# Optimization experiments

Hardware: AMD Instinct MI355X
Metric: run time of the kernel (lower is better)

The kernel has to match this reference:

```python
import math
import jax, jax.numpy as jnp
import numpy as np

DIM = 1024
FFN_DIM = 4096
NUM_HEADS = 16
HEAD_DIM = DIM // NUM_HEADS
SCALE = 1.0 / math.sqrt(HEAD_DIM)
EPS = 1e-5


def _layer_norm(x, gamma, beta):
    mu = jnp.mean(x, axis=-1, keepdims=True)
    var = jnp.mean(jnp.square(x - mu), axis=-1, keepdims=True)
    return (x - mu) * jax.lax.rsqrt(var + EPS) * gamma + beta


def _gelu_erf(x):
    # matches torch GELU module: x * 0.5 * (1 + erf(x / sqrt(2)))
    return x * 0.5 * (1.0 + jax.lax.erf(x / math.sqrt(2.0)))


def setup_inputs() -> dict:
    key = jax.random.key(0)
    ks = jax.random.split(key, 12)
    B, L = 2, 2048
    s = 0.02
    inp = {
        "x": jax.random.normal(ks[0], (B, L, DIM), dtype=jnp.float32),
        "g1": jnp.ones((DIM,), jnp.float32),
        "b1": jnp.zeros((DIM,), jnp.float32),
        "Wq": jax.random.normal(ks[1], (DIM, DIM), jnp.float32) * s,
        "bq": jnp.zeros((DIM,), jnp.float32),
        "Wk": jax.random.normal(ks[2], (DIM, DIM), jnp.float32) * s,
        "bk": jnp.zeros((DIM,), jnp.float32),
        "Wv": jax.random.normal(ks[3], (DIM, DIM), jnp.float32) * s,
        "bv": jnp.zeros((DIM,), jnp.float32),
        "Wo": jax.random.normal(ks[4], (DIM, DIM), jnp.float32) * s,
        "bo": jnp.zeros((DIM,), jnp.float32),
        "g2": jnp.ones((DIM,), jnp.float32),
        "b2": jnp.zeros((DIM,), jnp.float32),
        "W1": jax.random.normal(ks[5], (FFN_DIM, DIM), jnp.float32) * s,
        "bf1": jnp.zeros((FFN_DIM,), jnp.float32),
        "W2": jax.random.normal(ks[6], (DIM, FFN_DIM), jnp.float32) * s,
        "bf2": jnp.zeros((DIM,), jnp.float32),
    }
    return inp


def reference(x, g1, b1, Wq, bq, Wk, bk, Wv, bv, Wo, bo, g2, b2, W1, bf1, W2, bf2):
    B, L, C = x.shape
    n, c = NUM_HEADS, HEAD_DIM

    # ---- pre-norm self-attention ----
    h = _layer_norm(x, g1, b1)
    q = (h @ Wq.T + bq).reshape(B, L, n, c)
    k = (h @ Wk.T + bk).reshape(B, L, n, c)
    v = (h @ Wv.T + bv).reshape(B, L, n, c)
    attn = SCALE * jnp.einsum('binc,bjnc->bnij', q, k)   # [B, n, L, L]
    attn = jax.nn.softmax(attn, axis=-1)
    o = jnp.einsum('bnij,bjnc->binc', attn, v).reshape(B, L, C)
    x = x + (o @ Wo.T + bo)

    # ---- pre-norm FFN (GELU, erf form) ----
    h = _layer_norm(x, g2, b2)
    h = _gelu_erf(h @ W1.T + bf1)
    x = x + (h @ W2.T + bf2)
    return x
```

## Files before the change

### kernel.cpp

```cpp
#include <hip/hip_runtime.h>
#include <hip/hip_bf16.h>
#include <math.h>

typedef unsigned short u16;
typedef __attribute__((ext_vector_type(8))) __bf16 bf16x8;
typedef __attribute__((ext_vector_type(4))) float f32x4;

#define DIM   1024
#define LSEQ  2048
#define BTOK  4096
#define HD    64
#define FFN   4096
#define QSCL  0.18033688011112042f

#if __has_builtin(__builtin_amdgcn_exp2f)
#define EXP2(x) __builtin_amdgcn_exp2f(x)
#else
#define EXP2(x) exp2f(x)
#endif

__device__ __forceinline__ u16 f2bf(float f) {
  unsigned u = __builtin_bit_cast(unsigned, f);
  u += 0x7FFFu + ((u >> 16) & 1u);
  return (u16)(u >> 16);
}
__device__ __forceinline__ unsigned pk2(float a, float b) {
  return (unsigned)f2bf(a) | ((unsigned)f2bf(b) << 16);
}
__device__ __forceinline__ unsigned cvtpk(float lo, float hi) {
  unsigned r;
  asm("v_cvt_pk_bf16_f32 %0, %1, %2" : "=v"(r) : "v"(lo), "v"(hi));
  return r;
}
__device__ __forceinline__ f32x4 mfma16(bf16x8 a, bf16x8 b, f32x4 c) {
  return __builtin_amdgcn_mfma_f32_16x16x32_bf16(a, b, c, 0, 0, 0);
}
__device__ __forceinline__ void gload16(const void* g, void* l) {
  __builtin_amdgcn_global_load_lds((const __attribute__((address_space(1))) char*)g,
                                   (__attribute__((address_space(3))) char*)l, 16, 0, 0);
}
__device__ __forceinline__ float gelu_t(float v) {
  float v3 = v * v * v;
  float tt = fmaf(-0.10296766f, v3, -2.30258509f * v);
  return v * __builtin_amdgcn_rcpf(1.0f + EXP2(tt));
}

__global__ __launch_bounds__(256) void ln_kernel(const float* __restrict__ x,
                                                 const float* __restrict__ g,
                                                 const float* __restrict__ bta,
                                                 u16* __restrict__ out) {
  int row = blockIdx.x, t = threadIdx.x;
  const float* xr = x + (size_t)row * DIM;
  float4 xv = *(const float4*)(xr + t * 4);
  float s  = xv.x + xv.y + xv.z + xv.w;
  float ss = xv.x * xv.x + xv.y * xv.y + xv.z * xv.z + xv.w * xv.w;
#pragma unroll
  for (int m = 32; m >= 1; m >>= 1) {
    s  += __shfl_xor(s, m);
    ss += __shfl_xor(ss, m);
  }
  __shared__ float red[8];
  if ((t & 63) == 0) { red[(t >> 6) * 2] = s; red[(t >> 6) * 2 + 1] = ss; }
  __syncthreads();
  s  = red[0] + red[2] + red[4] + red[6];
  ss = red[1] + red[3] + red[5] + red[7];
  float mu  = s * (1.0f / DIM);
  float var = ss * (1.0f / DIM) - mu * mu;
  float rs  = rsqrtf(var + 1e-5f);
  float4 gv = *(const float4*)(g + t * 4);
  float4 bv = *(const float4*)(bta + t * 4);
  uint2 o;
  o.x = pk2((xv.x - mu) * rs * gv.x + bv.x, (xv.y - mu) * rs * gv.y + bv.y);
  o.y = pk2((xv.z - mu) * rs * gv.z + bv.z, (xv.w - mu) * rs * gv.w + bv.w);
  *(uint2*)(out + (size_t)row * DIM + t * 4) = o;
}

__global__ __launch_bounds__(256) void wcvt4(const float* __restrict__ Wq, const float* __restrict__ Wk,
                                             const float* __restrict__ Wv, const float* __restrict__ Wo,
                                             u16* __restrict__ dst) {
  int b = blockIdx.x;
  int r = b >> 9;
  const float* s = (r == 0) ? Wq : (r == 1) ? Wk : (r == 2) ? Wv : Wo;
  size_t i = (((size_t)(b & 511)) * 256 + threadIdx.x) * 8;
  float4 f0 = *(const float4*)(s + i), f1 = *(const float4*)(s + i + 4);
  uint4 o = { pk2(f0.x, f0.y), pk2(f0.z, f0.w), pk2(f1.x, f1.y), pk2(f1.z, f1.w) };
  *(uint4*)(dst + ((size_t)r << 20) + i) = o;
}
__global__ __launch_bounds__(256) void wcvt2(const float* __restrict__ W1, const float* __restrict__ W2,
                                             u16* __restrict__ d1, u16* __restrict__ d2) {
  int b = blockIdx.x;
  const float* s = (b < 2048) ? W1 : W2;
  u16* d = (b < 2048) ? d1 : d2;
  size_t i = (((size_t)(b & 2047)) * 256 + threadIdx.x) * 8;
  float4 f0 = *(const float4*)(s + i), f1 = *(const float4*)(s + i + 4);
  uint4 o = { pk2(f0.x, f0.y), pk2(f0.z, f0.w), pk2(f1.x, f1.y), pk2(f1.z, f1.w) };
  *(uint4*)(d + i) = o;
}

__global__ __launch_bounds__(256) void transpose_v(const u16* __restrict__ v,
                                                   u16* __restrict__ vt) {
  __shared__ u16 tls[64][80];
  int jb = blockIdx.x, bh = blockIdx.y, b = bh >> 4, h = bh & 15;
  int t = threadIdx.x;
  int r = t >> 2, seg = t & 3;
  const u16* src = v + (size_t)(b * LSEQ + jb * 64 + r) * DIM + h * HD + seg * 16;
  *(uint4*)&tls[r][seg * 16]     = *(const uint4*)src;
  *(uint4*)&tls[r][seg * 16 + 8] = *(const uint4*)(src + 8);
  __syncthreads();
  int c = t >> 2, jseg = t & 3;
  u16 tmp[16] __attribute__((aligned(16)));
#pragma unroll
  for (int i = 0; i < 16; i++) tmp[i] = tls[jseg * 16 + i][c];
  u16* dst = vt + ((size_t)bh * HD + c) * LSEQ + jb * 64 + jseg * 16;
  *(uint4*)dst       = *(const uint4*)tmp;
  *(uint4*)(dst + 8) = *(const uint4*)(tmp + 8);
}

struct GArg { const u16* Wb; const float* bias; u16* outB; float oscale; };

template <int EPI, int BM>
__global__ __launch_bounds__(256) void gemm3(const u16* __restrict__ A,
                                             GArg g0, GArg g1, GArg g2,
                                             const float* __restrict__ resid,
                                             float* __restrict__ outF,
                                             int N, int K, int nbPerW) {
  constexpr int WM = BM / 32;
  constexpr int ABUF = BM * 64;
  __shared__ u16 lsa[2][BM * 32];
  __shared__ u16 lsb[2][128 * 32];
  const int t = threadIdx.x;
  const int w = t >> 6, l = t & 63, l15 = l & 15, lg = l >> 4;
  const int wr = w >> 1, wc = w & 1;
  const int nwg = gridDim.x * gridDim.y;
  int flat = blockIdx.y * gridDim.x + blockIdx.x;
  flat = (flat & 7) * (nwg >> 3) + (flat >> 3);
  const int bx = flat % gridDim.x, by = flat / gridDim.x;
  const int sel = bx / nbPerW, nb = bx % nbPerW;
  GArg G = (sel == 0) ? g0 : ((sel == 1) ? g1 : g2);
  const int n0 = nb * 128, m0 = by * BM;

  f32x4 acc[WM][4];
#pragma unroll
  for (int m = 0; m < WM; m++)
#pragma unroll
    for (int n = 0; n < 4; n++) acc[m][n] = (f32x4){0.f, 0.f, 0.f, 0.f};

  const int grow = t >> 2;
  const int gcol = 8 * ((t & 3) ^ ((t >> 3) & 3));
  const u16* Asrc = A + (size_t)(m0 + grow) * K + gcol;
  const u16* Bsrc = G.Wb + (size_t)(n0 + grow) * K + gcol;
  const int rs = (l15 >> 1) & 3;

  const char* aadr = (const char*)lsa + (wr * (BM / 2) + l15) * 64 + (lg ^ rs) * 16;
  const char* badr = (const char*)lsb + (wc * 64 + l15) * 64 + (lg ^ rs) * 16;

  auto stage = [&](int k0, int buf) {
#pragma unroll
    for (int i = 0; i < BM / 64; i++)
      gload16(Asrc + (size_t)i * 64 * K + k0, (char*)lsa + buf * ABUF + i * 4096 + w * 1024);
#pragma unroll
    for (int i = 0; i < 2; i++)
      gload16(Bsrc + (size_t)i * 64 * K + k0, (char*)lsb + buf * 8192 + i * 4096 + w * 1024);
  };

  stage(0, 0);
  const int NT = K >> 5;
  for (int it = 0; it < NT; it++) {
    const int buf = it & 1;
    __syncthreads();
    if (it + 1 < NT) stage((it + 1) << 5, buf ^ 1);

    const char* ap = aadr + buf * ABUF;
    const char* bp = badr + buf * 8192;
    bf16x8 af[WM], bfr[4];
#pragma unroll
    for (int m = 0; m < WM; m++)
      af[m] = *(const bf16x8*)(ap + m * 1024);
#pragma unroll
    for (int n = 0; n < 4; n++)
      bfr[n] = *(const bf16x8*)(bp + n * 1024);
#pragma unroll
    for (int m = 0; m < WM; m++)
#pragma unroll
      for (int n = 0; n < 4; n++)
        acc[m][n] = mfma16(af[m], bfr[n], acc[m][n]);
  }

#pragma unroll
  for (int m = 0; m < WM; m++) {
    const int row = m0 + wr * (BM / 2) + m * 16 + lg * 4;
#pragma unroll
    for (int n = 0; n < 4; n++) {
      const int col = n0 + wc * 64 + n * 16 + l15;
      const float bias = G.bias[col];
#pragma unroll
      for (int r = 0; r < 4; r++) {
        const float v = acc[m][n][r] + bias;
        const size_t idx = (size_t)(row + r) * N + col;
        if (EPI == 0)      G.outB[idx] = f2bf(v * G.oscale);
        else if (EPI == 1) outF[idx] = v + resid[idx];
        else               G.outB[idx] = f2bf(gelu_t(v));
      }
    }
  }
}

__global__ __launch_bounds__(256, 4) void attn5(const u16* __restrict__ q,
                                                const u16* __restrict__ k,
                                                const u16* __restrict__ vt,
                                                u16* __restrict__ o) {
  __shared__ __align__(16) char smem[40960];
  const int t = threadIdx.x, w = t >> 6, l = t & 63, l15 = l & 15, lg = l >> 4;
  int flat = blockIdx.y * gridDim.x + blockIdx.x;
  flat = (flat & 7) * 128 + (flat >> 3);
  const int qbk = flat & 31, bh = flat >> 5;
  const int b = bh >> 4, h = bh & 15;
  const int qrow0 = b * LSEQ + qbk * 64 + w * 16;
  const int r7 = l15 & 7;
  const int c0 = lg ^ r7;

  bf16x8 av[2];
#pragma unroll
  for (int i = 0; i < 2; i++)
    av[i] = *(const bf16x8*)(q + (size_t)(qrow0 + l15) * DIM + h * HD + i * 32 + lg * 8);

  const char* adrA  = smem + l15 * 128 + c0 * 16;
  const char* adrB  = smem + l15 * 128 + (c0 ^ 4) * 16;
  const char* padrA = smem + 32768 + w * 2048 + l15 * 128 + c0 * 16;
  const char* padrB = smem + 32768 + w * 2048 + l15 * 128 + (c0 ^ 4) * 16;
  char* pwa[4];
#pragma unroll
  for (int cb = 0; cb < 4; cb++)
    pwa[cb] = smem + 32768 + w * 2048 + l15 * 128 +
              (((2 * cb + (lg >> 1)) ^ r7) * 16) + (lg & 1) * 8;

  const int grow = t >> 3, gchk = t & 7;
  const u16* ksrc = k + (size_t)(b * LSEQ + grow) * DIM + h * HD + 8 * (gchk ^ (grow & 7));
  const u16* vsrc = vt + ((size_t)bh * HD + grow) * LSEQ + 8 * (gchk ^ (grow & 7));

  f32x4 oacc[4];
#pragma unroll
  for (int cb = 0; cb < 4; cb++) oacc[cb] = (f32x4){0.f, 0.f, 0.f, 0.f};
  f32x4 minit = (f32x4){0.f, 0.f, 0.f, 0.f};
  float lsum = 0.f;

  auto issueTile = [&](int jt, int buf) {
    const u16* kp = ksrc + (size_t)jt * DIM;
    const u16* vp = vsrc + jt;
#pragma unroll
    for (int i = 0; i < 2; i++) {
      gload16(kp + (size_t)i * 32 * DIM,  smem + buf * 8192 + i * 4096 + w * 1024);
      gload16(vp + (size_t)i * 32 * LSEQ, smem + 16384 + buf * 8192 + i * 4096 + w * 1024);
    }
  };

  issueTile(0, 0);
  for (int it = 0; it < LSEQ / 64; it++) {
    const int buf = it & 1;
    __syncthreads();
    if (it + 1 < LSEQ / 64) issueTile((it + 1) * 64, buf ^ 1);
    const int ko = buf * 8192;

    f32x4 s[4];
    const char* kA = adrA + ko;
    const char* kB = adrB + ko;
    __builtin_amdgcn_s_setprio(1);
#pragma unroll
    for (int cb = 0; cb < 4; cb++) {
      bf16x8 kf0 = *(const bf16x8*)(kA + cb * 2048);
      bf16x8 kf1 = *(const bf16x8*)(kB + cb * 2048);
      s[cb] = mfma16(kf0, av[0], minit);
      s[cb] = mfma16(kf1, av[1], s[cb]);
    }
    __builtin_amdgcn_s_setprio(0);

    float tm = fmaxf(fmaxf(fmaxf(s[0][0], s[0][1]), fmaxf(s[0][2], s[0][3])),
                     fmaxf(fmaxf(fmaxf(s[1][0], s[1][1]), fmaxf(s[1][2], s[1][3])),
                           fmaxf(fmaxf(fmaxf(s[2][0], s[2][1]), fmaxf(s[2][2], s[2][3])),
                                 fmaxf(fmaxf(s[3][0], s[3][1]), fmaxf(s[3][2], s[3][3])))));
    if (__any(tm > 8.0f)) {
      float tr = fmaxf(tm, __shfl_xor(tm, 16));
      tr = fmaxf(tr, __shfl_xor(tr, 32));
      const float d = fmaxf(tr, 0.f);
      const float scl = EXP2(-d);
      const f32x4 dv = (f32x4){d, d, d, d};
      lsum *= scl;
      minit -= dv;
#pragma unroll
      for (int cb = 0; cb < 4; cb++) s[cb] -= dv;
#pragma unroll
      for (int r = 0; r < 4; r++) {
        const float so = __shfl(scl, lg * 4 + r);
#pragma unroll
        for (int cb = 0; cb < 4; cb++) oacc[cb][r] *= so;
      }
    }
    float ps = 0.f;
    uint2 pk[4];
#pragma unroll
    for (int cb = 0; cb < 4; cb++) {
      float a0 = EXP2(s[cb][0]);
      float a1 = EXP2(s[cb][1]);
      float a2 = EXP2(s[cb][2]);
      float a3 = EXP2(s[cb][3]);
      ps += (a0 + a1) + (a2 + a3);
      pk[cb].x = cvtpk(a0, a1);
      pk[cb].y = cvtpk(a2, a3);
    }
    lsum += ps;
#pragma unroll
    for (int cb = 0; cb < 4; cb++) *(uint2*)pwa[cb] = pk[cb];

    const char* vA = adrA + ko + 16384;
    const char* vB = adrB + ko + 16384;
    bf16x8 pa0 = *(const bf16x8*)padrA;
    bf16x8 pa1 = *(const bf16x8*)padrB;
    __builtin_amdgcn_s_setprio(1);
#pragma unroll
    for (int cb = 0; cb < 4; cb++) {
      bf16x8 vf0 = *(const bf16x8*)(vA + cb * 2048);
      oacc[cb] = mfma16(pa0, vf0, oacc[cb]);
    }
#pragma unroll
    for (int cb = 0; cb < 4; cb++) {
      bf16x8 vf1 = *(const bf16x8*)(vB + cb * 2048);
      oacc[cb] = mfma16(pa1, vf1, oacc[cb]);
    }
    __builtin_amdgcn_s_setprio(0);
  }

  float rl = lsum + __shfl_xor(lsum, 16);
  rl += __shfl_xor(rl, 32);
#pragma unroll
  for (int r = 0; r < 4; r++) {
    const float lo = __shfl(rl, lg * 4 + r);
    const float rcp = 1.0f / lo;
#pragma unroll
    for (int cb = 0; cb < 4; cb++) {
      o[(size_t)(qrow0 + lg * 4 + r) * DIM + h * HD + cb * 16 + l15] =
          f2bf(oacc[cb][r] * rcp);
    }
  }
}

extern "C" void kernel_launch(void* const* d_in, const int* in_sizes, int n_in,
                              void* d_out, int out_size, void* d_ws, size_t ws_size,
                              hipStream_t stream) {
  const float* x   = (const float*)d_in[0];
  const float* g1  = (const float*)d_in[1];
  const float* b1  = (const float*)d_in[2];
  const float* Wq  = (const float*)d_in[3];
  const float* bq  = (const float*)d_in[4];
  const float* Wk  = (const float*)d_in[5];
  const float* bk  = (const float*)d_in[6];
  const float* Wv  = (const float*)d_in[7];
  const float* bv  = (const float*)d_in[8];
  const float* Wo  = (const float*)d_in[9];
  const float* bo  = (const float*)d_in[10];
  const float* g2  = (const float*)d_in[11];
  const float* b2  = (const float*)d_in[12];
  const float* W1  = (const float*)d_in[13];
  const float* bf1 = (const float*)d_in[14];
  const float* W2  = (const float*)d_in[15];
  const float* bf2 = (const float*)d_in[16];
  float* out = (float*)d_out;

  const size_t E = (size_t)BTOK * DIM;
  u16* h     = (u16*)d_ws;
  u16* qb    = h + E;
  u16* kbuf  = qb + E;
  u16* vbuf  = kbuf + E;
  u16* vtb   = vbuf + E;
  u16* wqkvo = vtb + E;
  u16* ob    = vbuf;
  u16* W1b   = qb;
  u16* W2b   = kbuf;
  u16* mid   = vbuf;
  u16* h2    = h;
  float* x2  = out;

  u16* Wqb = wqkvo;
  u16* Wkb = wqkvo + ((size_t)1 << 20);
  u16* Wvb = wqkvo + ((size_t)2 << 20);
  u16* Wob = wqkvo + ((size_t)3 << 20);

  wcvt4<<<dim3(2048), dim3(256), 0, stream>>>(Wq, Wk, Wv, Wo, wqkvo);
  ln_kernel<<<dim3(BTOK), dim3(256), 0, stream>>>(x, g1, b1, h);
  gemm3<0, 128><<<dim3(24, BTOK / 128), 256, 0, stream>>>(
      h, GArg{Wqb, bq, qb, QSCL}, GArg{Wkb, bk, kbuf, 1.0f}, GArg{Wvb, bv, vbuf, 1.0f},
      nullptr, nullptr, DIM, DIM, 8);
  transpose_v<<<dim3(32, 32), 256, 0, stream>>>(vbuf, vtb);
  attn5<<<dim3(LSEQ / 64, 32), 256, 0, stream>>>(qb, kbuf, vtb, ob);
  {
    GArg s{Wob, bo, nullptr, 1.0f};
    gemm3<1, 64><<<dim3(8, BTOK / 64), 256, 0, stream>>>(ob, s, s, s, x, x2, DIM, DIM, 8);
  }
  wcvt2<<<dim3(4096), dim3(256), 0, stream>>>(W1, W2, W1b, W2b);
  ln_kernel<<<dim3(BTOK), dim3(256), 0, stream>>>(x2, g2, b2, h2);
  {
    GArg s{W1b, bf1, mid, 1.0f};
    gemm3<2, 128><<<dim3(32, BTOK / 128), 256, 0, stream>>>(h2, s, s, s, nullptr, nullptr, FFN, DIM, 32);
  }
  {
    GArg s{W2b, bf2, nullptr, 1.0f};
    gemm3<1, 64><<<dim3(8, BTOK / 64), 256, 0, stream>>>(mid, s, s, s, x2, out, DIM, FFN, 8);
  }
}
```

Measured before the change: 255.0 us.

## Deepen GEMM shared-memory pipeline to multi-stage with explicit vmcnt waits

```diff
diff --git a/kernel.cpp b/kernel.cpp
--- a/kernel.cpp
+++ b/kernel.cpp
@@ -118,16 +118,19 @@
 
 struct GArg { const u16* Wb; const float* bias; u16* outB; float oscale; };
 
-template <int EPI, int BM>
-__global__ __launch_bounds__(256) void gemm3(const u16* __restrict__ A,
+template <int EPI, int BM, int DEPTH>
+__global__ __launch_bounds__(256) void gemm4(const u16* __restrict__ A,
                                              GArg g0, GArg g1, GArg g2,
                                              const float* __restrict__ resid,
                                              float* __restrict__ outF,
                                              int N, int K, int nbPerW) {
-  constexpr int WM = BM / 32;
+  constexpr int WM  = BM / 32;
+  constexpr int LPT = BM / 64 + 2;
   constexpr int ABUF = BM * 64;
-  __shared__ u16 lsa[2][BM * 32];
-  __shared__ u16 lsb[2][128 * 32];
+  constexpr int BBUF = 8192;
+  constexpr int VX  = (DEPTH - 2) * LPT;
+  __shared__ u16 lsa[DEPTH][BM * 32];
+  __shared__ u16 lsb[DEPTH][128 * 32];
   const int t = threadIdx.x;
   const int w = t >> 6, l = t & 63, l15 = l & 15, lg = l >> 4;
   const int wr = w >> 1, wc = w & 1;
@@ -160,18 +163,23 @@
       gload16(Asrc + (size_t)i * 64 * K + k0, (char*)lsa + buf * ABUF + i * 4096 + w * 1024);
 #pragma unroll
     for (int i = 0; i < 2; i++)
-      gload16(Bsrc + (size_t)i * 64 * K + k0, (char*)lsb + buf * 8192 + i * 4096 + w * 1024);
+      gload16(Bsrc + (size_t)i * 64 * K + k0, (char*)lsb + buf * BBUF + i * 4096 + w * 1024);
   };
 
-  stage(0, 0);
+#pragma unroll
+  for (int p = 0; p < DEPTH - 1; p++) stage(p << 5, p);
+
   const int NT = K >> 5;
+  int bufR = 0, bufW = DEPTH - 1;
   for (int it = 0; it < NT; it++) {
-    const int buf = it & 1;
-    __syncthreads();
-    if (it + 1 < NT) stage((it + 1) << 5, buf ^ 1);
-
-    const char* ap = aadr + buf * ABUF;
-    const char* bp = badr + buf * 8192;
+    if constexpr (VX == 4) asm volatile("s_waitcnt vmcnt(4)" ::: "memory");
+    else if constexpr (VX == 6) asm volatile("s_waitcnt vmcnt(6)" ::: "memory");
+    else asm volatile("s_waitcnt vmcnt(0)" ::: "memory");
+    __builtin_amdgcn_s_barrier();
+    if (it + DEPTH - 1 < NT) stage((it + DEPTH - 1) << 5, bufW);
+
+    const char* ap = aadr + bufR * ABUF;
+    const char* bp = badr + bufR * BBUF;
     bf16x8 af[WM], bfr[4];
 #pragma unroll
     for (int m = 0; m < WM; m++)
@@ -179,11 +187,15 @@
 #pragma unroll
     for (int n = 0; n < 4; n++)
       bfr[n] = *(const bf16x8*)(bp + n * 1024);
+    __builtin_amdgcn_s_setprio(1);
 #pragma unroll
     for (int m = 0; m < WM; m++)
 #pragma unroll
       for (int n = 0; n < 4; n++)
         acc[m][n] = mfma16(af[m], bfr[n], acc[m][n]);
+    __builtin_amdgcn_s_setprio(0);
+    bufR = (bufR + 1 == DEPTH) ? 0 : bufR + 1;
+    bufW = (bufW + 1 == DEPTH) ? 0 : bufW + 1;
   }
 
 #pragma unroll
@@ -386,23 +398,23 @@
 
   wcvt4<<<dim3(2048), dim3(256), 0, stream>>>(Wq, Wk, Wv, Wo, wqkvo);
   ln_kernel<<<dim3(BTOK), dim3(256), 0, stream>>>(x, g1, b1, h);
-  gemm3<0, 128><<<dim3(24, BTOK / 128), 256, 0, stream>>>(
+  gemm4<0, 128, 3><<<dim3(24, BTOK / 128), 256, 0, stream>>>(
       h, GArg{Wqb, bq, qb, QSCL}, GArg{Wkb, bk, kbuf, 1.0f}, GArg{Wvb, bv, vbuf, 1.0f},
       nullptr, nullptr, DIM, DIM, 8);
   transpose_v<<<dim3(32, 32), 256, 0, stream>>>(vbuf, vtb);
   attn5<<<dim3(LSEQ / 64, 32), 256, 0, stream>>>(qb, kbuf, vtb, ob);
   {
     GArg s{Wob, bo, nullptr, 1.0f};
-    gemm3<1, 64><<<dim3(8, BTOK / 64), 256, 0, stream>>>(ob, s, s, s, x, x2, DIM, DIM, 8);
+    gemm4<1, 64, 4><<<dim3(8, BTOK / 64), 256, 0, stream>>>(ob, s, s, s, x, x2, DIM, DIM, 8);
   }
   wcvt2<<<dim3(4096), dim3(256), 0, stream>>>(W1, W2, W1b, W2b);
   ln_kernel<<<dim3(BTOK), dim3(256), 0, stream>>>(x2, g2, b2, h2);
   {
     GArg s{W1b, bf1, mid, 1.0f};
-    gemm3<2, 128><<<dim3(32, BTOK / 128), 256, 0, stream>>>(h2, s, s, s, nullptr, nullptr, FFN, DIM, 32);
+    gemm4<2, 128, 3><<<dim3(32, BTOK / 128), 256, 0, stream>>>(h2, s, s, s, nullptr, nullptr, FFN, DIM, 32);
   }
   {
     GArg s{W2b, bf2, nullptr, 1.0f};
-    gemm3<1, 64><<<dim3(8, BTOK / 64), 256, 0, stream>>>(mid, s, s, s, x2, out, DIM, FFN, 8);
-  }
-}
+    gemm4<1, 64, 4><<<dim3(8, BTOK / 64), 256, 0, stream>>>(mid, s, s, s, x2, out, DIM, FFN, 8);
+  }
+}
```

Result: no change. 258.7 us (+1.5%).

## Give each attention wave 32 query rows, halving waves per block

Applied to the files above, without the earlier changes.

```diff
diff --git a/kernel.cpp b/kernel.cpp
--- a/kernel.cpp
+++ b/kernel.cpp
@@ -205,7 +205,7 @@
   }
 }
 
-__global__ __launch_bounds__(256, 4) void attn5(const u16* __restrict__ q,
+__global__ __launch_bounds__(128, 2) void attn6(const u16* __restrict__ q,
                                                 const u16* __restrict__ k,
                                                 const u16* __restrict__ vt,
                                                 u16* __restrict__ o) {
@@ -215,42 +215,47 @@
   flat = (flat & 7) * 128 + (flat >> 3);
   const int qbk = flat & 31, bh = flat >> 5;
   const int b = bh >> 4, h = bh & 15;
-  const int qrow0 = b * LSEQ + qbk * 64 + w * 16;
+  const int qrow0 = b * LSEQ + qbk * 64 + w * 32;
   const int r7 = l15 & 7;
   const int c0 = lg ^ r7;
 
-  bf16x8 av[2];
-#pragma unroll
-  for (int i = 0; i < 2; i++)
-    av[i] = *(const bf16x8*)(q + (size_t)(qrow0 + l15) * DIM + h * HD + i * 32 + lg * 8);
+  bf16x8 av[2][2];
+#pragma unroll
+  for (int m = 0; m < 2; m++)
+#pragma unroll
+    for (int i = 0; i < 2; i++)
+      av[m][i] = *(const bf16x8*)(q + (size_t)(qrow0 + m * 16 + l15) * DIM + h * HD + i * 32 + lg * 8);
 
   const char* adrA  = smem + l15 * 128 + c0 * 16;
   const char* adrB  = smem + l15 * 128 + (c0 ^ 4) * 16;
-  const char* padrA = smem + 32768 + w * 2048 + l15 * 128 + c0 * 16;
-  const char* padrB = smem + 32768 + w * 2048 + l15 * 128 + (c0 ^ 4) * 16;
+  const char* padrA = smem + 32768 + w * 4096 + l15 * 128 + c0 * 16;
+  const char* padrB = smem + 32768 + w * 4096 + l15 * 128 + (c0 ^ 4) * 16;
   char* pwa[4];
 #pragma unroll
   for (int cb = 0; cb < 4; cb++)
-    pwa[cb] = smem + 32768 + w * 2048 + l15 * 128 +
+    pwa[cb] = smem + 32768 + w * 4096 + l15 * 128 +
               (((2 * cb + (lg >> 1)) ^ r7) * 16) + (lg & 1) * 8;
 
-  const int grow = t >> 3, gchk = t & 7;
-  const u16* ksrc = k + (size_t)(b * LSEQ + grow) * DIM + h * HD + 8 * (gchk ^ (grow & 7));
-  const u16* vsrc = vt + ((size_t)bh * HD + grow) * LSEQ + 8 * (gchk ^ (grow & 7));
-
-  f32x4 oacc[4];
-#pragma unroll
-  for (int cb = 0; cb < 4; cb++) oacc[cb] = (f32x4){0.f, 0.f, 0.f, 0.f};
-  f32x4 minit = (f32x4){0.f, 0.f, 0.f, 0.f};
-  float lsum = 0.f;
+  const int srow = l >> 3;
+  const int schk = 8 * ((l & 7) ^ (srow & 7));
+  const u16* ksrc = k + (size_t)(b * LSEQ + w * 32 + srow) * DIM + h * HD + schk;
+  const u16* vsrc = vt + ((size_t)bh * HD + w * 32 + srow) * LSEQ + schk;
+
+  f32x4 oacc[2][4];
+#pragma unroll
+  for (int m = 0; m < 2; m++)
+#pragma unroll
+    for (int cb = 0; cb < 4; cb++) oacc[m][cb] = (f32x4){0.f, 0.f, 0.f, 0.f};
+  f32x4 minit[2] = {(f32x4){0.f, 0.f, 0.f, 0.f}, (f32x4){0.f, 0.f, 0.f, 0.f}};
+  float lsum[2] = {0.f, 0.f};
 
   auto issueTile = [&](int jt, int buf) {
     const u16* kp = ksrc + (size_t)jt * DIM;
     const u16* vp = vsrc + jt;
 #pragma unroll
-    for (int i = 0; i < 2; i++) {
-      gload16(kp + (size_t)i * 32 * DIM,  smem + buf * 8192 + i * 4096 + w * 1024);
-      gload16(vp + (size_t)i * 32 * LSEQ, smem + 16384 + buf * 8192 + i * 4096 + w * 1024);
+    for (int j = 0; j < 4; j++) {
+      gload16(kp + (size_t)j * 8 * DIM,  smem + buf * 8192 + w * 4096 + j * 1024);
+      gload16(vp + (size_t)j * 8 * LSEQ, smem + 16384 + buf * 8192 + w * 4096 + j * 1024);
     }
   };
 
@@ -261,7 +266,7 @@
     if (it + 1 < LSEQ / 64) issueTile((it + 1) * 64, buf ^ 1);
     const int ko = buf * 8192;
 
-    f32x4 s[4];
+    f32x4 s[2][4];
     const char* kA = adrA + ko;
     const char* kB = adrB + ko;
     __builtin_amdgcn_s_setprio(1);
@@ -269,76 +274,96 @@
     for (int cb = 0; cb < 4; cb++) {
       bf16x8 kf0 = *(const bf16x8*)(kA + cb * 2048);
       bf16x8 kf1 = *(const bf16x8*)(kB + cb * 2048);
-      s[cb] = mfma16(kf0, av[0], minit);
-      s[cb] = mfma16(kf1, av[1], s[cb]);
+      s[0][cb] = mfma16(kf0, av[0][0], minit[0]);
+      s[1][cb] = mfma16(kf0, av[1][0], minit[1]);
+      s[0][cb] = mfma16(kf1, av[0][1], s[0][cb]);
+      s[1][cb] = mfma16(kf1, av[1][1], s[1][cb]);
     }
     __builtin_amdgcn_s_setprio(0);
 
-    float tm = fmaxf(fmaxf(fmaxf(s[0][0], s[0][1]), fmaxf(s[0][2], s[0][3])),
-                     fmaxf(fmaxf(fmaxf(s[1][0], s[1][1]), fmaxf(s[1][2], s[1][3])),
-                           fmaxf(fmaxf(fmaxf(s[2][0], s[2][1]), fmaxf(s[2][2], s[2][3])),
-                                 fmaxf(fmaxf(s[3][0], s[3][1]), fmaxf(s[3][2], s[3][3])))));
-    if (__any(tm > 8.0f)) {
-      float tr = fmaxf(tm, __shfl_xor(tm, 16));
-      tr = fmaxf(tr, __shfl_xor(tr, 32));
-      const float d = fmaxf(tr, 0.f);
-      const float scl = EXP2(-d);
-      const f32x4 dv = (f32x4){d, d, d, d};
-      lsum *= scl;
-      minit -= dv;
-#pragma unroll
-      for (int cb = 0; cb < 4; cb++) s[cb] -= dv;
-#pragma unroll
-      for (int r = 0; r < 4; r++) {
-        const float so = __shfl(scl, lg * 4 + r);
-#pragma unroll
-        for (int cb = 0; cb < 4; cb++) oacc[cb][r] *= so;
+    float tm[2];
+#pragma unroll
+    for (int m = 0; m < 2; m++)
+      tm[m] = fmaxf(fmaxf(fmaxf(s[m][0][0], s[m][0][1]), fmaxf(s[m][0][2], s[m][0][3])),
+                    fmaxf(fmaxf(fmaxf(s[m][1][0], s[m][1][1]), fmaxf(s[m][1][2], s[m][1][3])),
+                          fmaxf(fmaxf(fmaxf(s[m][2][0], s[m][2][1]), fmaxf(s[m][2][2], s[m][2][3])),
+                                fmaxf(fmaxf(s[m][3][0], s[m][3][1]), fmaxf(s[m][3][2], s[m][3][3])))));
+    if (__any(fmaxf(tm[0], tm[1]) > 8.0f)) {
+#pragma unroll
+      for (int m = 0; m < 2; m++) {
+        float tr = fmaxf(tm[m], __shfl_xor(tm[m], 16));
+        tr = fmaxf(tr, __shfl_xor(tr, 32));
+        const float d = fmaxf(tr, 0.f);
+        const float scl = EXP2(-d);
+        const f32x4 dv = (f32x4){d, d, d, d};
+        lsum[m] *= scl;
+        minit[m] -= dv;
+#pragma unroll
+        for (int cb = 0; cb < 4; cb++) s[m][cb] -= dv;
+#pragma unroll
+        for (int r = 0; r < 4; r++) {
+          const float so = __shfl(scl, lg * 4 + r);
+#pragma unroll
+          for (int cb = 0; cb < 4; cb++) oacc[m][cb][r] *= so;
+        }
       }
     }
-    float ps = 0.f;
-    uint2 pk[4];
-#pragma unroll
-    for (int cb = 0; cb < 4; cb++) {
-      float a0 = EXP2(s[cb][0]);
-      float a1 = EXP2(s[cb][1]);
-      float a2 = EXP2(s[cb][2]);
-      float a3 = EXP2(s[cb][3]);
-      ps += (a0 + a1) + (a2 + a3);
-      pk[cb].x = cvtpk(a0, a1);
-      pk[cb].y = cvtpk(a2, a3);
-    }
-    lsum += ps;
-#pragma unroll
-    for (int cb = 0; cb < 4; cb++) *(uint2*)pwa[cb] = pk[cb];
+#pragma unroll
+    for (int m = 0; m < 2; m++) {
+      float ps = 0.f;
+      uint2 pk[4];
+#pragma unroll
+      for (int cb = 0; cb < 4; cb++) {
+        float a0 = EXP2(s[m][cb][0]);
+        float a1 = EXP2(s[m][cb][1]);
+        float a2 = EXP2(s[m][cb][2]);
+        float a3 = EXP2(s[m][cb][3]);
+        ps += (a0 + a1) + (a2 + a3);
+        pk[cb].x = cvtpk(a0, a1);
+        pk[cb].y = cvtpk(a2, a3);
+      }
+      lsum[m] += ps;
+#pragma unroll
+      for (int cb = 0; cb < 4; cb++) *(uint2*)(pwa[cb] + m * 2048) = pk[cb];
+    }
 
     const char* vA = adrA + ko + 16384;
     const char* vB = adrB + ko + 16384;
-    bf16x8 pa0 = *(const bf16x8*)padrA;
-    bf16x8 pa1 = *(const bf16x8*)padrB;
+    bf16x8 pa0[2], pa1[2];
+#pragma unroll
+    for (int m = 0; m < 2; m++) {
+      pa0[m] = *(const bf16x8*)(padrA + m * 2048);
+      pa1[m] = *(const bf16x8*)(padrB + m * 2048);
+    }
     __builtin_amdgcn_s_setprio(1);
 #pragma unroll
     for (int cb = 0; cb < 4; cb++) {
       bf16x8 vf0 = *(const bf16x8*)(vA + cb * 2048);
-      oacc[cb] = mfma16(pa0, vf0, oacc[cb]);
+      oacc[0][cb] = mfma16(pa0[0], vf0, oacc[0][cb]);
+      oacc[1][cb] = mfma16(pa0[1], vf0, oacc[1][cb]);
     }
 #pragma unroll
     for (int cb = 0; cb < 4; cb++) {
       bf16x8 vf1 = *(const bf16x8*)(vB + cb * 2048);
-      oacc[cb] = mfma16(pa1, vf1, oacc[cb]);
+      oacc[0][cb] = mfma16(pa1[0], vf1, oacc[0][cb]);
+      oacc[1][cb] = mfma16(pa1[1], vf1, oacc[1][cb]);
     }
     __builtin_amdgcn_s_setprio(0);
   }
 
-  float rl = lsum + __shfl_xor(lsum, 16);
-  rl += __shfl_xor(rl, 32);
-#pragma unroll
-  for (int r = 0; r < 4; r++) {
-    const float lo = __shfl(rl, lg * 4 + r);
-    const float rcp = 1.0f / lo;
-#pragma unroll
-    for (int cb = 0; cb < 4; cb++) {
-      o[(size_t)(qrow0 + lg * 4 + r) * DIM + h * HD + cb * 16 + l15] =
-          f2bf(oacc[cb][r] * rcp);
+#pragma unroll
+  for (int m = 0; m < 2; m++) {
+    float rl = lsum[m] + __shfl_xor(lsum[m], 16);
+    rl += __shfl_xor(rl, 32);
+#pragma unroll
+    for (int r = 0; r < 4; r++) {
+      const float lo = __shfl(rl, lg * 4 + r);
+      const float rcp = 1.0f / lo;
+#pragma unroll
+      for (int cb = 0; cb < 4; cb++) {
+        o[(size_t)(qrow0 + m * 16 + lg * 4 + r) * DIM + h * HD + cb * 16 + l15] =
+            f2bf(oacc[m][cb][r] * rcp);
+      }
     }
   }
 }
@@ -390,7 +415,7 @@
       h, GArg{Wqb, bq, qb, QSCL}, GArg{Wkb, bk, kbuf, 1.0f}, GArg{Wvb, bv, vbuf, 1.0f},
       nullptr, nullptr, DIM, DIM, 8);
   transpose_v<<<dim3(32, 32), 256, 0, stream>>>(vbuf, vtb);
-  attn5<<<dim3(LSEQ / 64, 32), 256, 0, stream>>>(qb, kbuf, vtb, ob);
+  attn6<<<dim3(LSEQ / 64, 32), 128, 0, stream>>>(qb, kbuf, vtb, ob);
   {
     GArg s{Wob, bo, nullptr, 1.0f};
     gemm3<1, 64><<<dim3(8, BTOK / 64), 256, 0, stream>>>(ob, s, s, s, x, x2, DIM, DIM, 8);
```

After: 254.5 us. About the same (-0.2%).
